# Performance work log

Hardware: AMD Instinct MI355X
Metric: run time of the kernel (lower is better)

## Reference

```python
import jax, jax.numpy as jnp
import numpy as np

B, L, H = 4, 1024, 1024
NH, HD = 16, 64
ND = NH * HD
ITERS = 4
U = 5  # MSA1 ring window size (hard-coded in source)


def _conv1x1(w, b, x):  # w [O,C], b [O], x [B,C,L] -> [B,O,L]  (Conv2d 1x1 == per-position linear)
    return jnp.einsum('oc,bcl->bol', w, x) + b[None, :, None]


def _layernorm(x, s, b, eps=1e-5):  # x [B,H,L]; LayerNorm over channel dim H
    mu = x.mean(1, keepdims=True)
    var = ((x - mu) ** 2).mean(1, keepdims=True)
    return (x - mu) / jnp.sqrt(var + eps) * s[None, :, None] + b[None, :, None]


def _msa1(x, ax, wq, bq, wk, bk, wv, bv, wo, bo):
    # x [B,H,L] normalized nodes; ax [B,H,2,L] (ring embedding + relay)
    b, h, l = x.shape
    q = _conv1x1(wq, bq, x).reshape(b, NH, HD, l)
    k = _conv1x1(wk, bk, x).reshape(b, NH, HD, l)
    v = _conv1x1(wv, bv, x).reshape(b, NH, HD, l)
    pad = U // 2
    kp = jnp.pad(k, ((0, 0), (0, 0), (0, 0), (pad, pad)))
    vp = jnp.pad(v, ((0, 0), (0, 0), (0, 0), (pad, pad)))
    # F.unfold with (U,1) kernel along L == stack of U shifted views
    kw = jnp.stack([kp[..., u:u + l] for u in range(U)], axis=3)  # [B,NH,HD,U,L]
    vw = jnp.stack([vp[..., u:u + l] for u in range(U)], axis=3)
    al = ax.shape[2]
    ak = (jnp.einsum('oc,bcal->boal', wk, ax) + bk[None, :, None, None]).reshape(b, NH, HD, al, l)
    av = (jnp.einsum('oc,bcal->boal', wv, ax) + bv[None, :, None, None]).reshape(b, NH, HD, al, l)
    kw = jnp.concatenate([kw, ak], axis=3)  # [B,NH,HD,U+2,L]
    vw = jnp.concatenate([vw, av], axis=3)
    scores = (q[:, :, :, None, :] * kw).sum(2) / np.sqrt(HD)  # [B,NH,U+2,L]
    alphas = jax.nn.softmax(scores, axis=2)
    att = (alphas[:, :, None, :, :] * vw).sum(3).reshape(b, ND, l)
    return _conv1x1(wo, bo, att)  # [B,H,L]


def _msa2(relay, y, smask, wq, bq, wk, bk, wo, bo):
    # relay [B,H]; y [B,H,L+1]; smask [B,L+1] True at padding
    b = relay.shape[0]
    q = (jnp.einsum('oc,bc->bo', wq, relay) + bq).reshape(b, NH, HD)
    k = _conv1x1(wk, bk, y).reshape(b, NH, HD, -1)
    pre = jnp.einsum('bnd,bndl->bnl', q, k) / np.sqrt(HD)
    pre = jnp.where(smask[:, None, :], -1e10, pre)
    alphas = jax.nn.softmax(pre, axis=-1)
    # NOTE: source has v = k (WV output unused) -- reproduced faithfully
    att = jnp.einsum('bnl,bndl->bnd', alphas, k).reshape(b, ND)
    return jnp.einsum('oc,bc->bo', wo, att) + bo  # [B,H]


def _star_forward(data, mask, ln_s, ln_b, rwq, rwq_b, rwk, rwk_b, rwv, rwv_b, rwo, rwo_b,
                  swq, swq_b, swk, swk_b, swo, swo_b):
    b, l, h = data.shape
    pad_mask = (mask == 0)  # True at padding positions
    smask = jnp.concatenate([jnp.zeros((b, 1), bool), pad_mask], axis=1)  # [B,L+1]
    embs = jnp.transpose(data, (0, 2, 1))  # [B,H,L]
    nodes = embs
    relay = embs.mean(2)  # [B,H]
    for i in range(ITERS):
        xn = _layernorm(nodes, ln_s[i], ln_b[i])
        ax = jnp.stack([embs, jnp.broadcast_to(relay[:, :, None], embs.shape)], axis=2)  # [B,H,2,L]
        ring = _msa1(xn, ax, rwq[i], rwq_b[i], rwk[i], rwk_b[i], rwv[i], rwv_b[i], rwo[i], rwo_b[i])
        nodes = nodes + jax.nn.leaky_relu(ring)
        y = jnp.concatenate([relay[:, :, None], nodes], axis=2)  # [B,H,L+1]
        relay = jax.nn.leaky_relu(_msa2(relay, y, smask, swq[i], swq_b[i], swk[i], swk_b[i], swo[i], swo_b[i]))
        nodes = jnp.where(pad_mask[:, None, :], 0.0, nodes)
    return jnp.transpose(nodes, (0, 2, 1)), relay  # [B,L,H], [B,H]


def setup_inputs() -> dict:
    key = jax.random.key(0)
    ks = jax.random.split(key, 16)
    def p(k, shape):
        return jax.random.normal(k, shape, jnp.float32) * 0.02
    return dict(
        data=jax.random.normal(ks[0], (B, L, H), jnp.float32),
        mask=jax.random.randint(ks[1], (B, L), 0, 2).astype(jnp.int32),
        ln_s=jnp.ones((ITERS, H), jnp.float32),
        ln_b=jnp.zeros((ITERS, H), jnp.float32),
        rwq=p(ks[2], (ITERS, ND, H)), rwq_b=p(ks[3], (ITERS, ND)),
        rwk=p(ks[4], (ITERS, ND, H)), rwk_b=p(ks[5], (ITERS, ND)),
        rwv=p(ks[6], (ITERS, ND, H)), rwv_b=p(ks[7], (ITERS, ND)),
        rwo=p(ks[8], (ITERS, H, ND)), rwo_b=p(ks[9], (ITERS, H)),
        swq=p(ks[10], (ITERS, ND, H)), swq_b=p(ks[11], (ITERS, ND)),
        swk=p(ks[12], (ITERS, ND, H)), swk_b=p(ks[13], (ITERS, ND)),
        swo=p(ks[14], (ITERS, H, ND)), swo_b=p(ks[15], (ITERS, H)),
    )


def reference(data, mask, ln_s, ln_b, rwq, rwq_b, rwk, rwk_b, rwv, rwv_b, rwo, rwo_b,
              swq, swq_b, swk, swk_b, swo, swo_b):
    return _star_forward(data, mask, ln_s, ln_b, rwq, rwq_b, rwk, rwk_b, rwv, rwv_b,
                         rwo, rwo_b, swq, swq_b, swk, swk_b, swo, swo_b)
```

## Files before the change

kernel.cpp:

```cpp
#include <hip/hip_runtime.h>
#include <math.h>

namespace {

constexpr int B_ = 4, L_ = 1024, H_ = 1024, NH_ = 16, HD_ = 64, ND_ = 1024, ITERS_ = 4;

typedef unsigned short u16;
typedef __attribute__((ext_vector_type(8))) short short8;
typedef __attribute__((ext_vector_type(4))) float f32x4;

__device__ inline u16 f2bf(float f) {
  unsigned u = __builtin_bit_cast(unsigned, f);
  u += 0x7FFFu + ((u >> 16) & 1u);
  return (u16)(u >> 16);
}
__device__ inline float bf2f(u16 v) {
  unsigned u = ((unsigned)v) << 16;
  return __builtin_bit_cast(float, u);
}

__device__ inline void gl_lds16(const u16* g, u16* l) {
  __builtin_amdgcn_global_load_lds((const __attribute__((address_space(1))) void*)g,
                                   (__attribute__((address_space(3))) void*)l, 16, 0, 0);
}

__global__ void k_prep(const float* __restrict__ data, const float* __restrict__ rwq,
                       const float* __restrict__ rwk, const float* __restrict__ rwv,
                       const float* __restrict__ rwo, const float* __restrict__ swk,
                       u16* __restrict__ embs_bf, u16* __restrict__ wq_bf,
                       u16* __restrict__ wk_bf, u16* __restrict__ wv_bf,
                       u16* __restrict__ wo_bf, u16* __restrict__ swk_bf,
                       float* __restrict__ nodes) {
  int i = blockIdx.x * 256 + threadIdx.x;
  int which = blockIdx.y;
  if (which == 6) {
    reinterpret_cast<float4*>(nodes)[i] = reinterpret_cast<const float4*>(data)[i];
    return;
  }
  const float* src;
  u16* dst;
  switch (which) {
    case 0: src = data; dst = embs_bf; break;
    case 1: src = rwq; dst = wq_bf; break;
    case 2: src = rwk; dst = wk_bf; break;
    case 3: src = rwv; dst = wv_bf; break;
    case 4: src = rwo; dst = wo_bf; break;
    default: src = swk; dst = swk_bf; break;
  }
  float4 v = reinterpret_cast<const float4*>(src)[i];
  ushort4 o;
  o.x = f2bf(v.x); o.y = f2bf(v.y); o.z = f2bf(v.z); o.w = f2bf(v.w);
  reinterpret_cast<ushort4*>(dst)[i] = o;
}

__global__ void k_relay_part(const float* __restrict__ data, float* __restrict__ part) {
  int b = blockIdx.z, chunk = blockIdx.y;
  int c = blockIdx.x * 256 + threadIdx.x;
  const float* p = data + ((size_t)b * L_ + chunk * 128) * H_ + c;
  float acc = 0.f;
  for (int l = 0; l < 128; ++l) acc += p[(size_t)l * H_];
  part[((size_t)b * 8 + chunk) * H_ + c] = acc;
}
__global__ void k_relay_reduce(const float* __restrict__ part, float* __restrict__ relay) {
  int i = blockIdx.x * 256 + threadIdx.x;
  int b = i >> 10, c = i & 1023;
  float acc = 0.f;
  for (int j = 0; j < 8; ++j) acc += part[((size_t)b * 8 + j) * H_ + c];
  relay[i] = acc * (1.f / (float)L_);
}

__global__ __launch_bounds__(256) void k_layernorm_bf(float* __restrict__ nodes,
                                                      const float* __restrict__ s,
                                                      const float* __restrict__ bb,
                                                      const int* __restrict__ mask,
                                                      u16* __restrict__ y, int do_zero) {
  int row = blockIdx.x * 4 + (threadIdx.x >> 6);
  int lane = threadIdx.x & 63;
  int b = row >> 10, l = row & 1023;
  bool pad = do_zero && (mask[b * L_ + l] == 0);
  float4* xr = reinterpret_cast<float4*>(nodes + (size_t)row * H_);
  float4 v[4];
  float sum = 0.f, sq = 0.f;
#pragma unroll
  for (int j = 0; j < 4; ++j) {
    v[j] = pad ? float4{0.f, 0.f, 0.f, 0.f} : xr[lane + 64 * j];
    sum += v[j].x + v[j].y + v[j].z + v[j].w;
    sq += v[j].x * v[j].x + v[j].y * v[j].y + v[j].z * v[j].z + v[j].w * v[j].w;
  }
  if (pad) {
#pragma unroll
    for (int j = 0; j < 4; ++j) xr[lane + 64 * j] = float4{0.f, 0.f, 0.f, 0.f};
  }
#pragma unroll
  for (int off = 32; off; off >>= 1) {
    sum += __shfl_xor(sum, off);
    sq += __shfl_xor(sq, off);
  }
  float mu = sum * (1.f / (float)H_);
  float rstd = rsqrtf(sq * (1.f / (float)H_) - mu * mu + 1e-5f);
  ushort4* yr = reinterpret_cast<ushort4*>(y + (size_t)row * H_);
#pragma unroll
  for (int j = 0; j < 4; ++j) {
    int c4 = lane + 64 * j;
    float4 sc = reinterpret_cast<const float4*>(s)[c4];
    float4 bc = reinterpret_cast<const float4*>(bb)[c4];
    ushort4 o;
    o.x = f2bf((v[j].x - mu) * rstd * sc.x + bc.x);
    o.y = f2bf((v[j].y - mu) * rstd * sc.y + bc.y);
    o.z = f2bf((v[j].z - mu) * rstd * sc.z + bc.z);
    o.w = f2bf((v[j].w - mu) * rstd * sc.w + bc.w);
    yr[c4] = o;
  }
}


#define GEMM_PROLOGUE(XPTR, WPTR)                                              \
  __shared__ __align__(16) u16 sX[2][128 * 32];                                \
  __shared__ __align__(16) u16 sW[2][128 * 32];                                \
  const int t = threadIdx.x;                                                   \
  const int w = t >> 6, lane = t & 63;                                         \
  const int wm = w >> 1, wn = w & 1;                                           \
  const int r4 = lane >> 2, slot = lane & 3;                                   \
  const int rowS0 = w * 16 + r4, rowS1 = 64 + rowS0;                           \
  const int colS0 = ((slot ^ ((rowS0 >> 1) & 3)) << 3);                        \
  const int colS1 = ((slot ^ ((rowS1 >> 1) & 3)) << 3);                        \
  const u16* gX0 = (XPTR) + (size_t)(bm + rowS0) * 1024 + colS0;               \
  const u16* gX1 = (XPTR) + (size_t)(bm + rowS1) * 1024 + colS1;               \
  const u16* gW0 = (WPTR) + (size_t)(bn + rowS0) * 1024 + colS0;               \
  const u16* gW1 = (WPTR) + (size_t)(bn + rowS1) * 1024 + colS1;               \
  u16* lX0a = sX[0] + w * 512;                                                 \
  u16* lX0b = sX[1] + w * 512;                                                 \
  u16* lX1a = sX[0] + (4 + w) * 512;                                           \
  u16* lX1b = sX[1] + (4 + w) * 512;                                           \
  u16* lW0a = sW[0] + w * 512;                                                 \
  u16* lW0b = sW[1] + w * 512;                                                 \
  u16* lW1a = sW[0] + (4 + w) * 512;                                           \
  u16* lW1b = sW[1] + (4 + w) * 512;                                           \
  const int kidx = (((lane >> 4) ^ ((lane >> 1) & 3)) << 3);                   \
  f32x4 acc[4][4];                                                             \
  _Pragma("unroll") for (int i_ = 0; i_ < 4; ++i_)                             \
      _Pragma("unroll") for (int j_ = 0; j_ < 4; ++j_)                         \
          acc[i_][j_] = f32x4{0.f, 0.f, 0.f, 0.f};

#define GEMM_KLOOP64(AROWBASE, BROWBASE, ASRC, BSRC)                           \
  for (int ck = 0; ck < 1024; ck += 64) {                                      \
    gl_lds16(gX0, lX0a);                                                       \
    gl_lds16(gX0 + 32, lX0b);                                                  \
    gl_lds16(gX1, lX1a);                                                       \
    gl_lds16(gX1 + 32, lX1b);                                                  \
    gl_lds16(gW0, lW0a);                                                       \
    gl_lds16(gW0 + 32, lW0b);                                                  \
    gl_lds16(gW1, lW1a);                                                       \
    gl_lds16(gW1 + 32, lW1b);                                                  \
    gX0 += 64; gX1 += 64; gW0 += 64; gW1 += 64;                                \
    __syncthreads();                                                           \
    _Pragma("unroll") for (int h = 0; h < 2; ++h) {                            \
      short8 af_[4], bf_[4];                                                   \
      _Pragma("unroll") for (int mf = 0; mf < 4; ++mf)                         \
          af_[mf] = *reinterpret_cast<const short8*>(                          \
              &ASRC[h][((AROWBASE) + mf * 16) * 32 + kidx]);                   \
      _Pragma("unroll") for (int nf = 0; nf < 4; ++nf)                         \
          bf_[nf] = *reinterpret_cast<const short8*>(                          \
              &BSRC[h][((BROWBASE) + nf * 16) * 32 + kidx]);                   \
      _Pragma("unroll") for (int mf = 0; mf < 4; ++mf)                         \
          _Pragma("unroll") for (int nf = 0; nf < 4; ++nf)                     \
              acc[mf][nf] = __builtin_amdgcn_mfma_f32_16x16x32_bf16(           \
                  af_[mf], bf_[nf], acc[mf][nf], 0, 0, 0);                     \
    }                                                                          \
    __syncthreads();                                                          \
  }

__global__ __launch_bounds__(256, 3) void k_gemm5(const u16* __restrict__ wq,
                                                  const u16* __restrict__ wk,
                                                  const u16* __restrict__ wv,
                                                  const float* __restrict__ bq,
                                                  const float* __restrict__ bk,
                                                  const float* __restrict__ bv,
                                                  const u16* __restrict__ xn,
                                                  const u16* __restrict__ embs,
                                                  u16* __restrict__ Y) {
  const int bm = blockIdx.x * 128;
  const int which = blockIdx.y >> 3;
  const int bn = (blockIdx.y & 7) * 128;
  const u16* W = (which == 0) ? wq : ((which == 1 || which == 3) ? wk : wv);
  const float* bias = (which == 0) ? bq : ((which == 1 || which == 3) ? bk : bv);
  const u16* X = (which < 3) ? xn : embs;
  u16* Yw = Y + (size_t)which * ((size_t)B_ * L_ * ND_);

  GEMM_PROLOGUE(X, W)
  const int rW = wm * 64 + (lane & 15);
  const int rX = wn * 64 + (lane & 15);
  GEMM_KLOOP64(rW, rX, sW, sX)

#pragma unroll
  for (int mo = 0; mo < 4; ++mo) {
    int o0 = bn + wm * 64 + mo * 16 + ((lane >> 4) << 2);
    float4 bs = *reinterpret_cast<const float4*>(bias + o0);
#pragma unroll
    for (int nl = 0; nl < 4; ++nl) {
      int bl = bm + wn * 64 + nl * 16 + (lane & 15);
      f32x4 vv = acc[mo][nl];
      ushort4 ov;
      ov.x = f2bf(vv[0] + bs.x);
      ov.y = f2bf(vv[1] + bs.y);
      ov.z = f2bf(vv[2] + bs.z);
      ov.w = f2bf(vv[3] + bs.w);
      *reinterpret_cast<ushort4*>(&Yw[(size_t)bl * 1024 + o0]) = ov;
    }
  }
}


#define SMALL_PROLOGUE(XPTR, WPTR)                                             \
  __shared__ __align__(16) u16 sX[2][128 * 32];                                \
  __shared__ __align__(16) u16 sW[2][64 * 32];                                 \
  const int t = threadIdx.x;                                                   \
  const int w = t >> 6, lane = t & 63;                                         \
  const int wm = w >> 1, wn = w & 1;                                           \
  const int r4 = lane >> 2, slot = lane & 3;                                   \
  const int rowS0 = w * 16 + r4, rowS1 = 64 + rowS0;                           \
  const int colS0 = ((slot ^ ((rowS0 >> 1) & 3)) << 3);                        \
  const int colS1 = ((slot ^ ((rowS1 >> 1) & 3)) << 3);                        \
  const u16* gX0 = (XPTR) + (size_t)(bm + rowS0) * 1024 + colS0;               \
  const u16* gX1 = (XPTR) + (size_t)(bm + rowS1) * 1024 + colS1;               \
  const u16* gW0 = (WPTR) + (size_t)(bn + rowS0) * 1024 + colS0;               \
  u16* lX0a = sX[0] + w * 512;                                                 \
  u16* lX0b = sX[1] + w * 512;                                                 \
  u16* lX1a = sX[0] + (4 + w) * 512;                                           \
  u16* lX1b = sX[1] + (4 + w) * 512;                                           \
  u16* lW0a = sW[0] + w * 512;                                                 \
  u16* lW0b = sW[1] + w * 512;                                                 \
  const int kidx = (((lane >> 4) ^ ((lane >> 1) & 3)) << 3);

#define SMALL_KLOOP(MFN, NFN, ACC, AROWBASE, BROWBASE, ASRC, BSRC)             \
  for (int ck = 0; ck < 1024; ck += 64) {                                      \
    gl_lds16(gX0, lX0a);                                                       \
    gl_lds16(gX0 + 32, lX0b);                                                  \
    gl_lds16(gX1, lX1a);                                                       \
    gl_lds16(gX1 + 32, lX1b);                                                  \
    gl_lds16(gW0, lW0a);                                                       \
    gl_lds16(gW0 + 32, lW0b);                                                  \
    gX0 += 64; gX1 += 64; gW0 += 64;                                           \
    __syncthreads();                                                           \
    _Pragma("unroll") for (int h = 0; h < 2; ++h) {                            \
      short8 af_[MFN], bf_[NFN];                                               \
      _Pragma("unroll") for (int mf = 0; mf < MFN; ++mf)                       \
          af_[mf] = *reinterpret_cast<const short8*>(                          \
              &ASRC[h][((AROWBASE) + mf * 16) * 32 + kidx]);                   \
      _Pragma("unroll") for (int nf = 0; nf < NFN; ++nf)                       \
          bf_[nf] = *reinterpret_cast<const short8*>(                          \
              &BSRC[h][((BROWBASE) + nf * 16) * 32 + kidx]);                   \
      _Pragma("unroll") for (int mf = 0; mf < MFN; ++mf)                       \
          _Pragma("unroll") for (int nf = 0; nf < NFN; ++nf)                   \
              ACC[mf][nf] = __builtin_amdgcn_mfma_f32_16x16x32_bf16(           \
                  af_[mf], bf_[nf], ACC[mf][nf], 0, 0, 0);                     \
    }                                                                          \
    __syncthreads();                                                          \
  }

__global__ __launch_bounds__(256, 2) void k_gemm_wo_s(const u16* __restrict__ W,
                                                      const float* __restrict__ bias,
                                                      const u16* __restrict__ X,
                                                      float* __restrict__ nodes,
                                                      u16* __restrict__ nodes_bf) {
  const int bm = blockIdx.x * 128;
  const int bn = blockIdx.y * 64;
  SMALL_PROLOGUE(X, W)
  f32x4 acc[2][4];
#pragma unroll
  for (int i_ = 0; i_ < 2; ++i_)
#pragma unroll
    for (int j_ = 0; j_ < 4; ++j_) acc[i_][j_] = f32x4{0.f, 0.f, 0.f, 0.f};
  const int rW = wm * 32 + (lane & 15);
  const int rX = wn * 64 + (lane & 15);
  SMALL_KLOOP(2, 4, acc, rW, rX, sW, sX)

#pragma unroll
  for (int mo = 0; mo < 2; ++mo) {
    int o0 = bn + wm * 32 + mo * 16 + ((lane >> 4) << 2);
    float4 bs = *reinterpret_cast<const float4*>(bias + o0);
#pragma unroll
    for (int nl = 0; nl < 4; ++nl) {
      int bl = bm + wn * 64 + nl * 16 + (lane & 15);
      size_t ni = (size_t)bl * 1024 + o0;
      float4 curv = *reinterpret_cast<const float4*>(&nodes[ni]);
      f32x4 vv = acc[mo][nl];
      float r0 = vv[0] + bs.x; r0 = curv.x + (r0 > 0.f ? r0 : 0.01f * r0);
      float r1 = vv[1] + bs.y; r1 = curv.y + (r1 > 0.f ? r1 : 0.01f * r1);
      float r2 = vv[2] + bs.z; r2 = curv.z + (r2 > 0.f ? r2 : 0.01f * r2);
      float r3 = vv[3] + bs.w; r3 = curv.w + (r3 > 0.f ? r3 : 0.01f * r3);
      *reinterpret_cast<float4*>(&nodes[ni]) = float4{r0, r1, r2, r3};
      ushort4 ov;
      ov.x = f2bf(r0); ov.y = f2bf(r1); ov.z = f2bf(r2); ov.w = f2bf(r3);
      *reinterpret_cast<ushort4*>(&nodes_bf[ni]) = ov;
    }
  }
}

__global__ __launch_bounds__(256, 2) void k_gemm_kkb_s(const u16* __restrict__ W,
                                                       const float* __restrict__ bias,
                                                       const u16* __restrict__ X,
                                                       float* __restrict__ Y) {
  const int bm = blockIdx.x * 128;
  const int bn = blockIdx.y * 64;
  SMALL_PROLOGUE(X, W)
  f32x4 acc[4][2];
#pragma unroll
  for (int i_ = 0; i_ < 4; ++i_)
#pragma unroll
    for (int j_ = 0; j_ < 2; ++j_) acc[i_][j_] = f32x4{0.f, 0.f, 0.f, 0.f};
  const int rX = wm * 64 + (lane & 15);
  const int rW = wn * 32 + (lane & 15);
  SMALL_KLOOP(4, 2, acc, rX, rW, sX, sW)

#pragma unroll
  for (int nf = 0; nf < 2; ++nf) {
    int o = bn + wn * 32 + nf * 16 + (lane & 15);
    float bs = bias[o];
#pragma unroll
    for (int mf = 0; mf < 4; ++mf) {
      int gl = bm + wm * 64 + mf * 16 + ((lane >> 4) << 2);
      int b = gl >> 10, l = gl & 1023;
      size_t yi = ((size_t)(b * 1024 + o)) * (size_t)(L_ + 1) + 1 + l;
      f32x4 v = acc[mf][nf];
#pragma unroll
      for (int r = 0; r < 4; ++r) Y[yi + r] = v[r] + bs;
    }
  }
}

__global__ __launch_bounds__(256) void k_matvec4(const float* __restrict__ W0,
                                                 const float* __restrict__ b0, float* __restrict__ y0,
                                                 const float* __restrict__ W1,
                                                 const float* __restrict__ b1, float* __restrict__ y1,
                                                 const float* __restrict__ W2,
                                                 const float* __restrict__ b2, float* __restrict__ y2,
                                                 const float* __restrict__ W3,
                                                 const float* __restrict__ b3, float* __restrict__ y3,
                                                 long sB3, long sO3,
                                                 const float* __restrict__ x) {
  int b = blockIdx.y, z = blockIdx.z;
  const float* W = (z == 0) ? W0 : (z == 1) ? W1 : (z == 2) ? W2 : W3;
  const float* bias = (z == 0) ? b0 : (z == 1) ? b1 : (z == 2) ? b2 : b3;
  int o = blockIdx.x * 4 + (threadIdx.x >> 6);
  int lane = threadIdx.x & 63;
  const float* wr = W + (size_t)o * 1024;
  const float* xb = x + (size_t)b * 1024;
  float acc = 0.f;
  for (int c = lane; c < 1024; c += 64) acc += wr[c] * xb[c];
#pragma unroll
  for (int off = 32; off; off >>= 1) acc += __shfl_xor(acc, off);
  if (lane == 0) {
    acc += bias[o];
    if (z == 3) y3[(size_t)b * sB3 + (size_t)o * sO3] = acc;
    else if (z == 2) y2[(size_t)b * 1024 + o] = acc;
    else if (z == 1) y1[(size_t)b * 1024 + o] = acc;
    else y0[(size_t)b * 1024 + o] = acc;
  }
}

__global__ __launch_bounds__(256) void k_msa1(const u16* __restrict__ q,
                                              const u16* __restrict__ k,
                                              const u16* __restrict__ v,
                                              const u16* __restrict__ ke,
                                              const u16* __restrict__ ve,
                                              const float* __restrict__ rk,
                                              const float* __restrict__ rv,
                                              u16* __restrict__ attbf) {
  int t = threadIdx.x;
  int wv = t >> 6, lane = t & 63;
  int head = lane >> 2, dq = lane & 3;
  int l = blockIdx.x * 4 + wv;
  int b = blockIdx.z;
  size_t row = ((size_t)(b * 1024 + l)) * 1024 + head * 64 + dq * 16;
  size_t rbase = (size_t)b * 1024 + head * 64 + dq * 16;

  float qf[16];
  {
    const short8* qp = reinterpret_cast<const short8*>(q + row);
#pragma unroll
    for (int j = 0; j < 2; ++j) {
      short8 qv = qp[j];
#pragma unroll
      for (int e = 0; e < 8; ++e) qf[j * 8 + e] = bf2f((u16)qv[e]);
    }
  }
  float s[7];
#pragma unroll
  for (int u = 0; u < 5; ++u) {
    int lk = l + u - 2;
    float su = 0.f;
    if (lk >= 0 && lk < L_) {
      const short8* kp = reinterpret_cast<const short8*>(
          k + ((size_t)(b * 1024 + lk)) * 1024 + head * 64 + dq * 16);
#pragma unroll
      for (int j = 0; j < 2; ++j) {
        short8 kv = kp[j];
#pragma unroll
        for (int e = 0; e < 8; ++e) su = fmaf(qf[j * 8 + e], bf2f((u16)kv[e]), su);
      }
    }
    s[u] = su;
  }
  {
    float su = 0.f;
    const short8* kp = reinterpret_cast<const short8*>(ke + row);
#pragma unroll
    for (int j = 0; j < 2; ++j) {
      short8 kv = kp[j];
#pragma unroll
      for (int e = 0; e < 8; ++e) su = fmaf(qf[j * 8 + e], bf2f((u16)kv[e]), su);
    }
    s[5] = su;
  }
  {
    float su = 0.f;
    const float4* rp = reinterpret_cast<const float4*>(rk + rbase);
#pragma unroll
    for (int j = 0; j < 4; ++j) {
      float4 r4 = rp[j];
      su = fmaf(qf[j * 4 + 0], r4.x, su);
      su = fmaf(qf[j * 4 + 1], r4.y, su);
      su = fmaf(qf[j * 4 + 2], r4.z, su);
      su = fmaf(qf[j * 4 + 3], r4.w, su);
    }
    s[6] = su;
  }
#pragma unroll
  for (int u = 0; u < 7; ++u) {
    s[u] += __shfl_xor(s[u], 1);
    s[u] += __shfl_xor(s[u], 2);
  }
  float m = -1e30f;
#pragma unroll
  for (int u = 0; u < 7; ++u) {
    s[u] *= 0.125f;
    m = fmaxf(m, s[u]);
  }
  float e[7], tot = 0.f;
#pragma unroll
  for (int u = 0; u < 7; ++u) {
    e[u] = expf(s[u] - m);
    tot += e[u];
  }
  float inv = 1.f / tot;
#pragma unroll
  for (int u = 0; u < 7; ++u) e[u] *= inv;

  float av[16];
  {
    const float4* rp = reinterpret_cast<const float4*>(rv + rbase);
#pragma unroll
    for (int j = 0; j < 4; ++j) {
      float4 r4 = rp[j];
      av[j * 4 + 0] = e[6] * r4.x;
      av[j * 4 + 1] = e[6] * r4.y;
      av[j * 4 + 2] = e[6] * r4.z;
      av[j * 4 + 3] = e[6] * r4.w;
    }
  }
  {
    const short8* vp = reinterpret_cast<const short8*>(ve + row);
#pragma unroll
    for (int j = 0; j < 2; ++j) {
      short8 vvv = vp[j];
#pragma unroll
      for (int ee = 0; ee < 8; ++ee) av[j * 8 + ee] = fmaf(e[5], bf2f((u16)vvv[ee]), av[j * 8 + ee]);
    }
  }
#pragma unroll
  for (int u = 0; u < 5; ++u) {
    int lk = l + u - 2;
    if (lk >= 0 && lk < L_) {
      const short8* vp = reinterpret_cast<const short8*>(
          v + ((size_t)(b * 1024 + lk)) * 1024 + head * 64 + dq * 16);
#pragma unroll
      for (int j = 0; j < 2; ++j) {
        short8 vvv = vp[j];
#pragma unroll
        for (int ee = 0; ee < 8; ++ee) av[j * 8 + ee] = fmaf(e[u], bf2f((u16)vvv[ee]), av[j * 8 + ee]);
      }
    }
  }
  u16 ob[16];
#pragma unroll
  for (int j = 0; j < 16; ++j) ob[j] = f2bf(av[j]);
  uint4* d4 = reinterpret_cast<uint4*>(attbf + row);
  const uint4* s4 = reinterpret_cast<const uint4*>(ob);
  d4[0] = s4[0];
  d4[1] = s4[1];
}

__global__ __launch_bounds__(256) void k_msa2p(const float* __restrict__ rq,
                                               const float* __restrict__ kk,
                                               const int* __restrict__ mask,
                                               float* __restrict__ pw,
                                               float* __restrict__ pE) {
  int n = blockIdx.x, c = blockIdx.y, b = blockIdx.z;
  int tid = threadIdx.x;
  __shared__ float sq_[HD_];
  __shared__ float se[260];
  size_t rb = (size_t)(b * NH_ + n) * HD_;
  if (tid < HD_) sq_[tid] = rq[rb + tid];
  __syncthreads();
  const float* kb = kk + rb * (size_t)(L_ + 1);
  int p0 = c * 256;
  {
    int p = p0 + tid;
    float e;
    if (p > 0 && mask[b * L_ + p - 1] == 0) {
      e = 0.f;
    } else {
      float acc = 0.f;
      for (int d = 0; d < HD_; ++d) acc = fmaf(sq_[d], kb[(size_t)d * (L_ + 1) + p], acc);
      e = expf(acc * 0.125f);
    }
    se[tid] = e;
  }
  int nP = 256;
  if (c == 3) {
    nP = 257;
    if (tid == 0) {
      float e;
      if (mask[b * L_ + 1023] == 0) {
        e = 0.f;
      } else {
        float acc = 0.f;
        for (int d = 0; d < HD_; ++d) acc = fmaf(sq_[d], kb[(size_t)d * (L_ + 1) + 1024], acc);
        e = expf(acc * 0.125f);
      }
      se[256] = e;
    }
  }
  __syncthreads();
  int lane = tid & 63, w = tid >> 6;
  if (w == 0) {
    float E = 0.f;
    for (int i = lane; i < nP; i += 64) E += se[i];
#pragma unroll
    for (int off = 32; off; off >>= 1) E += __shfl_xor(E, off);
    if (lane == 0) pE[((size_t)(b * NH_ + n)) * 4 + c] = E;
  }
  for (int dd = 0; dd < 16; ++dd) {
    int d = w * 16 + dd;
    const float* kd = kb + (size_t)d * (L_ + 1) + p0;
    float a = 0.f;
    for (int i = lane; i < nP; i += 64) a = fmaf(se[i], kd[i], a);
#pragma unroll
    for (int off = 32; off; off >>= 1) a += __shfl_xor(a, off);
    if (lane == 0) pw[(((size_t)(b * NH_ + n)) * 4 + c) * HD_ + d] = a;
  }
}

__global__ __launch_bounds__(256) void k_msa2r_swo(const float* __restrict__ pw,
                                                   const float* __restrict__ pE,
                                                   const float* __restrict__ swo,
                                                   const float* __restrict__ swo_b,
                                                   float* __restrict__ relay) {
  int b = blockIdx.y;
  int tid = threadIdx.x;
  __shared__ float satt[1024];
#pragma unroll
  for (int j = 0; j < 4; ++j) {
    int idx = tid * 4 + j;
    int bn = b * 16 + (idx >> 6), d = idx & 63;
    float E = pE[bn * 4 + 0] + pE[bn * 4 + 1] + pE[bn * 4 + 2] + pE[bn * 4 + 3];
    float ws = pw[((size_t)bn * 4 + 0) * HD_ + d] + pw[((size_t)bn * 4 + 1) * HD_ + d] +
               pw[((size_t)bn * 4 + 2) * HD_ + d] + pw[((size_t)bn * 4 + 3) * HD_ + d];
    satt[idx] = ws / E;
  }
  __syncthreads();
  int o = blockIdx.x * 4 + (tid >> 6);
  int lane = tid & 63;
  const float* wr = swo + (size_t)o * 1024;
  float acc = 0.f;
  for (int c = lane; c < 1024; c += 64) acc = fmaf(wr[c], satt[c], acc);
#pragma unroll
  for (int off = 32; off; off >>= 1) acc += __shfl_xor(acc, off);
  if (lane == 0) {
    acc += swo_b[o];
    relay[(size_t)b * 1024 + o] = acc > 0.f ? acc : 0.01f * acc;
  }
}

__global__ void k_final(const float* __restrict__ nodes, const int* __restrict__ mask,
                        float* __restrict__ out) {
  int i = blockIdx.x * 256 + threadIdx.x;
  int row = i >> 8;
  int b = row >> 10, l = row & 1023;
  float4 v = (mask[b * L_ + l] == 0) ? float4{0.f, 0.f, 0.f, 0.f}
                                     : reinterpret_cast<const float4*>(nodes)[i];
  reinterpret_cast<float4*>(out)[i] = v;
}

__global__ void k_copy_relay(const float* __restrict__ relay, float* __restrict__ out) {
  int i = blockIdx.x * 256 + threadIdx.x;
  out[i] = relay[i];
}

}

extern "C" void kernel_launch(void* const* d_in, const int* in_sizes, int n_in,
                              void* d_out, int out_size, void* d_ws, size_t ws_size,
                              hipStream_t stream) {
  (void)in_sizes; (void)n_in; (void)out_size; (void)ws_size;
  const float* data = (const float*)d_in[0];
  const int* mask = (const int*)d_in[1];
  const float* ln_s = (const float*)d_in[2];
  const float* ln_b = (const float*)d_in[3];
  const float* rwq = (const float*)d_in[4];
  const float* rwq_b = (const float*)d_in[5];
  const float* rwk = (const float*)d_in[6];
  const float* rwk_b = (const float*)d_in[7];
  const float* rwv = (const float*)d_in[8];
  const float* rwv_b = (const float*)d_in[9];
  const float* rwo = (const float*)d_in[10];
  const float* rwo_b = (const float*)d_in[11];
  const float* swq = (const float*)d_in[12];
  const float* swq_b = (const float*)d_in[13];
  const float* swk = (const float*)d_in[14];
  const float* swk_b = (const float*)d_in[15];
  const float* swo = (const float*)d_in[16];
  const float* swo_b = (const float*)d_in[17];
  float* out = (float*)d_out;

  const size_t SZ = (size_t)B_ * ND_ * L_;
  float* f = (float*)d_ws;
  float* nodes = f; f += SZ;
  float* kkb = f; f += (size_t)B_ * ND_ * (L_ + 1);
  float* part = f; f += (size_t)B_ * 8 * H_;
  float* relay = f; f += B_ * H_;
  float* rk = f; f += B_ * ND_;
  float* rv = f; f += B_ * ND_;
  float* rq = f; f += B_ * ND_;
  float* pw = f; f += (size_t)B_ * NH_ * 4 * HD_;
  float* pE = f; f += B_ * NH_ * 4;
  u16* u = (u16*)f;
  u16* xn_bf = u; u += SZ;
  u16* embs_bf = u; u += SZ;
  u16* att_bf = u; u += SZ;
  u16* nodes_bf = u; u += SZ;
  u16* qkv5_bf = u; u += 5 * SZ;
  u16* wq_bf = u; u += SZ;
  u16* wk_bf = u; u += SZ;
  u16* wv_bf = u; u += SZ;
  u16* wo_bf = u; u += SZ;
  u16* swk_bf = u; u += SZ;

  k_prep<<<dim3(4096, 7), 256, 0, stream>>>(data, rwq, rwk, rwv, rwo, swk,
                                            embs_bf, wq_bf, wk_bf, wv_bf, wo_bf, swk_bf, nodes);
  k_relay_part<<<dim3(H_ / 256, 8, B_), 256, 0, stream>>>(data, part);
  k_relay_reduce<<<dim3((B_ * H_) / 256), 256, 0, stream>>>(part, relay);

  for (int i = 0; i < ITERS_; ++i) {
    const u16* wq_i = wq_bf + (size_t)i * ND_ * H_;
    const u16* wk_i = wk_bf + (size_t)i * ND_ * H_;
    const u16* wv_i = wv_bf + (size_t)i * ND_ * H_;
    const u16* wo_i = wo_bf + (size_t)i * H_ * ND_;
    const u16* sk_i = swk_bf + (size_t)i * ND_ * H_;

    k_layernorm_bf<<<dim3(B_ * L_ / 4), 256, 0, stream>>>(nodes, ln_s + i * H_, ln_b + i * H_,
                                                          mask, xn_bf, i > 0 ? 1 : 0);
    k_matvec4<<<dim3(256, B_, 4), 256, 0, stream>>>(
        rwk + (size_t)i * ND_ * H_, rwk_b + i * ND_, rk,
        rwv + (size_t)i * ND_ * H_, rwv_b + i * ND_, rv,
        swq + (size_t)i * ND_ * H_, swq_b + i * ND_, rq,
        swk + (size_t)i * ND_ * H_, swk_b + i * ND_, kkb, (long)ND_ * (L_ + 1), L_ + 1,
        relay);
    k_gemm5<<<dim3(32, 40), 256, 0, stream>>>(wq_i, wk_i, wv_i,
                                              rwq_b + i * ND_, rwk_b + i * ND_, rwv_b + i * ND_,
                                              xn_bf, embs_bf, qkv5_bf);
    k_msa1<<<dim3(L_ / 4, 1, B_), 256, 0, stream>>>(qkv5_bf, qkv5_bf + SZ, qkv5_bf + 2 * SZ,
                                                    qkv5_bf + 3 * SZ, qkv5_bf + 4 * SZ, rk, rv, att_bf);
    k_gemm_wo_s<<<dim3(32, 16), 256, 0, stream>>>(wo_i, rwo_b + i * H_, att_bf, nodes, nodes_bf);
    k_gemm_kkb_s<<<dim3(32, 16), 256, 0, stream>>>(sk_i, swk_b + i * ND_, nodes_bf, kkb);
    k_msa2p<<<dim3(NH_, 4, B_), 256, 0, stream>>>(rq, kkb, mask, pw, pE);
    k_msa2r_swo<<<dim3(256, B_), 256, 0, stream>>>(pw, pE, swo + (size_t)i * H_ * ND_,
                                                   swo_b + i * H_, relay);
  }
  k_final<<<4096, 256, 0, stream>>>(nodes, mask, out);
  k_copy_relay<<<dim3((B_ * H_) / 256), 256, 0, stream>>>(relay, out + (size_t)B_ * L_ * H_);
}
```

Before: 631.9 us.

## Store MSA2 keys position-major in bf16 and split MSA2 across positions

The star-key GEMM now writes its output as bf16 in a [B, L+1, ND] position-major layout instead of fp32 channel-major with stride L+1. The relay key row is also written in bf16. MSA2 is restructured into a position-parallel kernel that computes per-chunk exp-weighted sums with coalesced 16-channel loads, followed by a reduction kernel and a separate matvec for swo with leaky ReLU. This cuts key-buffer traffic and replaces strided per-head loops, at the cost of bf16 precision on keys, no max-subtraction in the softmax, and an extra kernel launch.

Result: faster. 618.0 us (median of 4 runs) (-2.2%).

```diff
diff --git a/kernel.cpp b/kernel.cpp
--- a/kernel.cpp
+++ b/kernel.cpp
@@ -297,34 +297,37 @@
   }
 }
 
-__global__ __launch_bounds__(256, 2) void k_gemm_kkb_s(const u16* __restrict__ W,
-                                                       const float* __restrict__ bias,
-                                                       const u16* __restrict__ X,
-                                                       float* __restrict__ Y) {
+__global__ __launch_bounds__(256, 2) void k_gemm_kkb_sw(const u16* __restrict__ W,
+                                                        const float* __restrict__ bias,
+                                                        const u16* __restrict__ X,
+                                                        u16* __restrict__ Y) {
   const int bm = blockIdx.x * 128;
   const int bn = blockIdx.y * 64;
   SMALL_PROLOGUE(X, W)
-  f32x4 acc[4][2];
-#pragma unroll
-  for (int i_ = 0; i_ < 4; ++i_)
-#pragma unroll
-    for (int j_ = 0; j_ < 2; ++j_) acc[i_][j_] = f32x4{0.f, 0.f, 0.f, 0.f};
-  const int rX = wm * 64 + (lane & 15);
-  const int rW = wn * 32 + (lane & 15);
-  SMALL_KLOOP(4, 2, acc, rX, rW, sX, sW)
-
-#pragma unroll
-  for (int nf = 0; nf < 2; ++nf) {
-    int o = bn + wn * 32 + nf * 16 + (lane & 15);
-    float bs = bias[o];
-#pragma unroll
-    for (int mf = 0; mf < 4; ++mf) {
-      int gl = bm + wm * 64 + mf * 16 + ((lane >> 4) << 2);
-      int b = gl >> 10, l = gl & 1023;
-      size_t yi = ((size_t)(b * 1024 + o)) * (size_t)(L_ + 1) + 1 + l;
-      f32x4 v = acc[mf][nf];
-#pragma unroll
-      for (int r = 0; r < 4; ++r) Y[yi + r] = v[r] + bs;
+  f32x4 acc[2][4];
+#pragma unroll
+  for (int i_ = 0; i_ < 2; ++i_)
+#pragma unroll
+    for (int j_ = 0; j_ < 4; ++j_) acc[i_][j_] = f32x4{0.f, 0.f, 0.f, 0.f};
+  const int rW = wm * 32 + (lane & 15);
+  const int rX = wn * 64 + (lane & 15);
+  SMALL_KLOOP(2, 4, acc, rW, rX, sW, sX)
+
+#pragma unroll
+  for (int mo = 0; mo < 2; ++mo) {
+    int o0 = bn + wm * 32 + mo * 16 + ((lane >> 4) << 2);
+    float4 bs = *reinterpret_cast<const float4*>(bias + o0);
+#pragma unroll
+    for (int nl = 0; nl < 4; ++nl) {
+      int bl = bm + wn * 64 + nl * 16 + (lane & 15);
+      size_t row = (size_t)(bl >> 10) * 1025 + 1 + (bl & 1023);
+      f32x4 vv = acc[mo][nl];
+      ushort4 ov;
+      ov.x = f2bf(vv[0] + bs.x);
+      ov.y = f2bf(vv[1] + bs.y);
+      ov.z = f2bf(vv[2] + bs.z);
+      ov.w = f2bf(vv[3] + bs.w);
+      *reinterpret_cast<ushort4*>(&Y[row * 1024 + o0]) = ov;
     }
   }
 }
@@ -336,8 +339,7 @@
                                                  const float* __restrict__ W2,
                                                  const float* __restrict__ b2, float* __restrict__ y2,
                                                  const float* __restrict__ W3,
-                                                 const float* __restrict__ b3, float* __restrict__ y3,
-                                                 long sB3, long sO3,
+                                                 const float* __restrict__ b3, u16* __restrict__ y3b,
                                                  const float* __restrict__ x) {
   int b = blockIdx.y, z = blockIdx.z;
   const float* W = (z == 0) ? W0 : (z == 1) ? W1 : (z == 2) ? W2 : W3;
@@ -352,10 +354,30 @@
   for (int off = 32; off; off >>= 1) acc += __shfl_xor(acc, off);
   if (lane == 0) {
     acc += bias[o];
-    if (z == 3) y3[(size_t)b * sB3 + (size_t)o * sO3] = acc;
+    if (z == 3) y3b[(size_t)b * 1025 * 1024 + o] = f2bf(acc);
     else if (z == 2) y2[(size_t)b * 1024 + o] = acc;
     else if (z == 1) y1[(size_t)b * 1024 + o] = acc;
     else y0[(size_t)b * 1024 + o] = acc;
+  }
+}
+
+__global__ __launch_bounds__(256) void k_matvec(const float* __restrict__ W,
+                                                const float* __restrict__ bias,
+                                                const float* __restrict__ x,
+                                                float* __restrict__ y, int leaky) {
+  int b = blockIdx.y;
+  int o = blockIdx.x * 4 + (threadIdx.x >> 6);
+  int lane = threadIdx.x & 63;
+  const float* wr = W + (size_t)o * 1024;
+  const float* xb = x + (size_t)b * 1024;
+  float acc = 0.f;
+  for (int c = lane; c < 1024; c += 64) acc += wr[c] * xb[c];
+#pragma unroll
+  for (int off = 32; off; off >>= 1) acc += __shfl_xor(acc, off);
+  if (lane == 0) {
+    acc += bias[o];
+    if (leaky) acc = acc > 0.f ? acc : 0.01f * acc;
+    y[(size_t)b * 1024 + o] = acc;
   }
 }
 
@@ -491,96 +513,71 @@
   d4[1] = s4[1];
 }
 
-__global__ __launch_bounds__(256) void k_msa2p(const float* __restrict__ rq,
-                                               const float* __restrict__ kk,
+__global__ __launch_bounds__(256) void k_msa2f(const u16* __restrict__ kkb,
+                                               const float* __restrict__ rq,
                                                const int* __restrict__ mask,
-                                               float* __restrict__ pw,
-                                               float* __restrict__ pE) {
-  int n = blockIdx.x, c = blockIdx.y, b = blockIdx.z;
-  int tid = threadIdx.x;
-  __shared__ float sq_[HD_];
-  __shared__ float se[260];
-  size_t rb = (size_t)(b * NH_ + n) * HD_;
-  if (tid < HD_) sq_[tid] = rq[rb + tid];
-  __syncthreads();
-  const float* kb = kk + rb * (size_t)(L_ + 1);
-  int p0 = c * 256;
+                                               float* __restrict__ avp,
+                                               float* __restrict__ Ep) {
+  int b = blockIdx.y;
+  int w = threadIdx.x >> 6, lane = threadIdx.x & 63;
+  int wc = blockIdx.x * 4 + w;
+  int q4 = lane & 3;
+  int ch0 = lane * 16;
+  float rqv[16];
   {
-    int p = p0 + tid;
-    float e;
-    if (p > 0 && mask[b * L_ + p - 1] == 0) {
-      e = 0.f;
-    } else {
-      float acc = 0.f;
-      for (int d = 0; d < HD_; ++d) acc = fmaf(sq_[d], kb[(size_t)d * (L_ + 1) + p], acc);
-      e = expf(acc * 0.125f);
-    }
-    se[tid] = e;
-  }
-  int nP = 256;
-  if (c == 3) {
-    nP = 257;
-    if (tid == 0) {
-      float e;
-      if (mask[b * L_ + 1023] == 0) {
-        e = 0.f;
-      } else {
-        float acc = 0.f;
-        for (int d = 0; d < HD_; ++d) acc = fmaf(sq_[d], kb[(size_t)d * (L_ + 1) + 1024], acc);
-        e = expf(acc * 0.125f);
-      }
-      se[256] = e;
-    }
-  }
-  __syncthreads();
-  int lane = tid & 63, w = tid >> 6;
-  if (w == 0) {
-    float E = 0.f;
-    for (int i = lane; i < nP; i += 64) E += se[i];
-#pragma unroll
-    for (int off = 32; off; off >>= 1) E += __shfl_xor(E, off);
-    if (lane == 0) pE[((size_t)(b * NH_ + n)) * 4 + c] = E;
-  }
-  for (int dd = 0; dd < 16; ++dd) {
-    int d = w * 16 + dd;
-    const float* kd = kb + (size_t)d * (L_ + 1) + p0;
-    float a = 0.f;
-    for (int i = lane; i < nP; i += 64) a = fmaf(se[i], kd[i], a);
-#pragma unroll
-    for (int off = 32; off; off >>= 1) a += __shfl_xor(a, off);
-    if (lane == 0) pw[(((size_t)(b * NH_ + n)) * 4 + c) * HD_ + d] = a;
-  }
-}
-
-__global__ __launch_bounds__(256) void k_msa2r_swo(const float* __restrict__ pw,
-                                                   const float* __restrict__ pE,
-                                                   const float* __restrict__ swo,
-                                                   const float* __restrict__ swo_b,
-                                                   float* __restrict__ relay) {
+    const float4* rp = reinterpret_cast<const float4*>(rq + (size_t)b * 1024 + ch0);
+#pragma unroll
+    for (int j = 0; j < 4; ++j) {
+      float4 v4 = rp[j];
+      rqv[j * 4 + 0] = v4.x; rqv[j * 4 + 1] = v4.y;
+      rqv[j * 4 + 2] = v4.z; rqv[j * 4 + 3] = v4.w;
+    }
+  }
+  float av[16];
+#pragma unroll
+  for (int j = 0; j < 16; ++j) av[j] = 0.f;
+  float eacc = 0.f;
+  int p0 = wc * 16;
+  int pend = p0 + 16;
+  if (pend > 1025) pend = 1025;
+  for (int p = p0; p < pend; ++p) {
+    if (p > 0 && mask[b * L_ + p - 1] == 0) continue;
+    const uint4* kr = reinterpret_cast<const uint4*>(kkb + ((size_t)b * 1025 + p) * 1024 + ch0);
+    uint4 ka = kr[0], kb2 = kr[1];
+    float kf[16];
+    const u16* kp = reinterpret_cast<const u16*>(&ka);
+#pragma unroll
+    for (int j = 0; j < 8; ++j) kf[j] = bf2f(kp[j]);
+    const u16* kp2 = reinterpret_cast<const u16*>(&kb2);
+#pragma unroll
+    for (int j = 0; j < 8; ++j) kf[8 + j] = bf2f(kp2[j]);
+    float s = 0.f;
+#pragma unroll
+    for (int j = 0; j < 16; ++j) s = fmaf(rqv[j], kf[j], s);
+    s += __shfl_xor(s, 1);
+    s += __shfl_xor(s, 2);
+    float e = expf(s * 0.125f);
+    if (q4 == 0) eacc += e;
+#pragma unroll
+    for (int j = 0; j < 16; ++j) av[j] = fmaf(e, kf[j], av[j]);
+  }
+  float* ap = avp + ((size_t)b * 68 + wc) * 1024 + ch0;
+#pragma unroll
+  for (int j = 0; j < 4; ++j)
+    reinterpret_cast<float4*>(ap)[j] =
+        float4{av[j * 4 + 0], av[j * 4 + 1], av[j * 4 + 2], av[j * 4 + 3]};
+  if (q4 == 0) Ep[((size_t)b * 68 + wc) * 16 + (lane >> 2)] = eacc;
+}
+
+__global__ void k_msa2r(const float* __restrict__ avp, const float* __restrict__ Ep,
+                        float* __restrict__ satt) {
   int b = blockIdx.y;
-  int tid = threadIdx.x;
-  __shared__ float satt[1024];
-#pragma unroll
-  for (int j = 0; j < 4; ++j) {
-    int idx = tid * 4 + j;
-    int bn = b * 16 + (idx >> 6), d = idx & 63;
-    float E = pE[bn * 4 + 0] + pE[bn * 4 + 1] + pE[bn * 4 + 2] + pE[bn * 4 + 3];
-    float ws = pw[((size_t)bn * 4 + 0) * HD_ + d] + pw[((size_t)bn * 4 + 1) * HD_ + d] +
-               pw[((size_t)bn * 4 + 2) * HD_ + d] + pw[((size_t)bn * 4 + 3) * HD_ + d];
-    satt[idx] = ws / E;
-  }
-  __syncthreads();
-  int o = blockIdx.x * 4 + (tid >> 6);
-  int lane = tid & 63;
-  const float* wr = swo + (size_t)o * 1024;
-  float acc = 0.f;
-  for (int c = lane; c < 1024; c += 64) acc = fmaf(wr[c], satt[c], acc);
-#pragma unroll
-  for (int off = 32; off; off >>= 1) acc += __shfl_xor(acc, off);
-  if (lane == 0) {
-    acc += swo_b[o];
-    relay[(size_t)b * 1024 + o] = acc > 0.f ? acc : 0.01f * acc;
-  }
+  int idx = blockIdx.x * 256 + threadIdx.x;
+  int head = idx >> 6;
+  float a = 0.f, E = 0.f;
+  for (int k = 0; k < 68; ++k) a += avp[((size_t)b * 68 + k) * 1024 + idx];
+  for (int k = 0; k < 68; ++k) E += Ep[((size_t)b * 68 + k) * 16 + head];
+  satt[(size_t)b * 1024 + idx] = a / E;
 }
 
 __global__ void k_final(const float* __restrict__ nodes, const int* __restrict__ mask,
@@ -627,19 +624,20 @@
   const size_t SZ = (size_t)B_ * ND_ * L_;
   float* f = (float*)d_ws;
   float* nodes = f; f += SZ;
-  float* kkb = f; f += (size_t)B_ * ND_ * (L_ + 1);
   float* part = f; f += (size_t)B_ * 8 * H_;
   float* relay = f; f += B_ * H_;
   float* rk = f; f += B_ * ND_;
   float* rv = f; f += B_ * ND_;
   float* rq = f; f += B_ * ND_;
-  float* pw = f; f += (size_t)B_ * NH_ * 4 * HD_;
-  float* pE = f; f += B_ * NH_ * 4;
+  float* satt = f; f += B_ * ND_;
+  float* avp = f; f += (size_t)B_ * 68 * 1024;
+  float* Ep = f; f += (size_t)B_ * 68 * 16;
   u16* u = (u16*)f;
   u16* xn_bf = u; u += SZ;
   u16* embs_bf = u; u += SZ;
   u16* att_bf = u; u += SZ;
   u16* nodes_bf = u; u += SZ;
+  u16* kkb_sw = u; u += (size_t)B_ * 1025 * 1024;
   u16* qkv5_bf = u; u += 5 * SZ;
   u16* wq_bf = u; u += SZ;
   u16* wk_bf = u; u += SZ;
@@ -665,18 +663,18 @@
         rwk + (size_t)i * ND_ * H_, rwk_b + i * ND_, rk,
         rwv + (size_t)i * ND_ * H_, rwv_b + i * ND_, rv,
         swq + (size_t)i * ND_ * H_, swq_b + i * ND_, rq,
-        swk + (size_t)i * ND_ * H_, swk_b + i * ND_, kkb, (long)ND_ * (L_ + 1), L_ + 1,
-        relay);
+        swk + (size_t)i * ND_ * H_, swk_b + i * ND_, kkb_sw, relay);
     k_gemm5<<<dim3(32, 40), 256, 0, stream>>>(wq_i, wk_i, wv_i,
                                               rwq_b + i * ND_, rwk_b + i * ND_, rwv_b + i * ND_,
                                               xn_bf, embs_bf, qkv5_bf);
     k_msa1<<<dim3(L_ / 4, 1, B_), 256, 0, stream>>>(qkv5_bf, qkv5_bf + SZ, qkv5_bf + 2 * SZ,
                                                     qkv5_bf + 3 * SZ, qkv5_bf + 4 * SZ, rk, rv, att_bf);
     k_gemm_wo_s<<<dim3(32, 16), 256, 0, stream>>>(wo_i, rwo_b + i * H_, att_bf, nodes, nodes_bf);
-    k_gemm_kkb_s<<<dim3(32, 16), 256, 0, stream>>>(sk_i, swk_b + i * ND_, nodes_bf, kkb);
-    k_msa2p<<<dim3(NH_, 4, B_), 256, 0, stream>>>(rq, kkb, mask, pw, pE);
-    k_msa2r_swo<<<dim3(256, B_), 256, 0, stream>>>(pw, pE, swo + (size_t)i * H_ * ND_,
-                                                   swo_b + i * H_, relay);
+    k_gemm_kkb_sw<<<dim3(32, 16), 256, 0, stream>>>(sk_i, swk_b + i * ND_, nodes_bf, kkb_sw);
+    k_msa2f<<<dim3(17, B_), 256, 0, stream>>>(kkb_sw, rq, mask, avp, Ep);
+    k_msa2r<<<dim3(4, B_), 256, 0, stream>>>(avp, Ep, satt);
+    k_matvec<<<dim3(256, B_), 256, 0, stream>>>(swo + (size_t)i * H_ * ND_, swo_b + i * H_,
+                                                satt, relay, 1);
   }
   k_final<<<4096, 256, 0, stream>>>(nodes, mask, out);
   k_copy_relay<<<dim3((B_ * H_) / 256), 256, 0, stream>>>(relay, out + (size_t)B_ * L_ * H_);
```
